# Kernel tuning notes

Hardware: AMD Instinct MI355X
Metric: run time of the kernel (lower is better)

The kernel has to match this reference:

```python
import jax, jax.numpy as jnp
import numpy as np

E = 1024      # embed_size
H = 16        # num_heads
DH = E // H   # head_size = 64
B = 4
T = 2048


def _layernorm(x, g, b, eps=1e-5):
    mu = jnp.mean(x, axis=-1, keepdims=True)
    var = jnp.var(x, axis=-1, keepdims=True)
    return (x - mu) * jax.lax.rsqrt(var + eps) * g + b


def setup_inputs() -> dict:
    key = jax.random.key(0)
    ks = jax.random.split(key, 12)
    s = 0.02
    return {
        "x": jax.random.normal(ks[0], (B, T, E), dtype=jnp.float32),
        "ln1_g": jnp.ones((E,), jnp.float32),
        "ln1_b": jnp.zeros((E,), jnp.float32),
        "Wq": jax.random.normal(ks[1], (H, E, DH), jnp.float32) * s,
        "Wk": jax.random.normal(ks[2], (H, E, DH), jnp.float32) * s,
        "Wv": jax.random.normal(ks[3], (H, E, DH), jnp.float32) * s,
        "Wp": jax.random.normal(ks[4], (E, E), jnp.float32) * s,
        "bp": jnp.zeros((E,), jnp.float32),
        "ln2_g": jnp.ones((E,), jnp.float32),
        "ln2_b": jnp.zeros((E,), jnp.float32),
        "W1": jax.random.normal(ks[5], (E, 4 * E), jnp.float32) * s,
        "b1": jnp.zeros((4 * E,), jnp.float32),
        "W2": jax.random.normal(ks[6], (4 * E, E), jnp.float32) * s,
        "b2": jnp.zeros((E,), jnp.float32),
    }


def reference(x, ln1_g, ln1_b, Wq, Wk, Wv, Wp, bp, ln2_g, ln2_b, W1, b1, W2, b2):
    # --- self-attention branch (pre-LN) ---
    h = _layernorm(x, ln1_g, ln1_b)
    q = jnp.einsum("bte,hed->bhtd", h, Wq)
    k = jnp.einsum("bte,hed->bhtd", h, Wk)
    v = jnp.einsum("bte,hed->bhtd", h, Wv)
    # NOTE: original scales by embed_size**-0.5 (C of the input), not head_size
    scale = jnp.float32(E) ** -0.5
    w = jnp.einsum("bhtd,bhsd->bhts", q, k) * scale  # [B,H,T,T]
    causal = jnp.tril(jnp.ones((T, T), dtype=bool))
    w = jnp.where(causal, w, -jnp.inf)
    w = jax.nn.softmax(w, axis=-1)
    att = jnp.einsum("bhts,bhsd->bhtd", w, v)        # [B,H,T,DH]
    att = jnp.transpose(att, (0, 2, 1, 3)).reshape(B, T, E)  # concat heads
    x = x + att @ Wp + bp
    # --- FFN branch (pre-LN) ---
    h2 = _layernorm(x, ln2_g, ln2_b)
    ff = jax.nn.relu(h2 @ W1 + b1) @ W2 + b2
    return x + ff
```

## Files before the change

### kernel.cpp

```cpp
#include <hip/hip_runtime.h>
#include <stdint.h>

#define DEV __device__ __forceinline__

typedef unsigned short u16;
typedef short s16x8 __attribute__((ext_vector_type(8)));
typedef u16 u16x4 __attribute__((ext_vector_type(4)));
typedef float f32x4 __attribute__((ext_vector_type(4)));

constexpr int Bc = 4, Tc = 2048, Ec = 1024, Hc = 16, DHc = 64, FFc = 4096;

DEV u16 f2bf(float f) {
    union { float f; uint32_t u; } v; v.f = f;
    uint32_t r = v.u + 0x7fffu + ((v.u >> 16) & 1u);
    return (u16)(r >> 16);
}
DEV float bf2f(u16 u) {
    union { uint32_t u; float f; } v; v.u = ((uint32_t)u) << 16;
    return v.f;
}

DEV void gload16(const void* g, void* l) {
    __builtin_amdgcn_global_load_lds((const __attribute__((address_space(1))) void*)g,
                                     (__attribute__((address_space(3))) void*)l, 16, 0, 0);
}

template <typename TIN>
__global__ __launch_bounds__(256) void transpose_conv(const TIN* __restrict__ in,
                                                      u16* __restrict__ out, int R, int C) {
    __shared__ float tile[32][33];
    int bz = blockIdx.z;
    in  += (size_t)bz * R * C;
    out += (size_t)bz * R * C;
    int c0 = blockIdx.x * 32, r0 = blockIdx.y * 32;
    int tx = threadIdx.x, ty = threadIdx.y;
#pragma unroll
    for (int i = 0; i < 4; i++) {
        int r = ty + 8 * i;
        float v;
        if constexpr (sizeof(TIN) == 4) v = ((const float*)in)[(size_t)(r0 + r) * C + c0 + tx];
        else                            v = bf2f(((const u16*)in)[(size_t)(r0 + r) * C + c0 + tx]);
        tile[r][tx] = v;
    }
    __syncthreads();
#pragma unroll
    for (int i = 0; i < 4; i++) {
        int c = ty + 8 * i;
        out[(size_t)(c0 + c) * R + r0 + tx] = f2bf(tile[tx][c]);
    }
}

__global__ __launch_bounds__(256) void ln_kernel(const float* __restrict__ x, const float* __restrict__ g,
                                                 const float* __restrict__ b, u16* __restrict__ out) {
    int row = blockIdx.x;
    const float4* xr = (const float4*)(x + (size_t)row * Ec);
    int t = threadIdx.x;
    float4 v = xr[t];
    float s = v.x + v.y + v.z + v.w;
    float ss = v.x * v.x + v.y * v.y + v.z * v.z + v.w * v.w;
#pragma unroll
    for (int off = 32; off > 0; off >>= 1) { s += __shfl_xor(s, off); ss += __shfl_xor(ss, off); }
    __shared__ float red[8];
    int wid = t >> 6;
    if ((t & 63) == 0) { red[wid] = s; red[4 + wid] = ss; }
    __syncthreads();
    s = red[0] + red[1] + red[2] + red[3];
    ss = red[4] + red[5] + red[6] + red[7];
    float mu = s * (1.f / Ec);
    float rs = rsqrtf(ss * (1.f / Ec) - mu * mu + 1e-5f);
    float4 gv = ((const float4*)g)[t], bv = ((const float4*)b)[t];
    u16x4 o;
    o[0] = f2bf((v.x - mu) * rs * gv.x + bv.x);
    o[1] = f2bf((v.y - mu) * rs * gv.y + bv.y);
    o[2] = f2bf((v.z - mu) * rs * gv.z + bv.z);
    o[3] = f2bf((v.w - mu) * rs * gv.w + bv.w);
    *(u16x4*)(out + (size_t)row * Ec + t * 4) = o;
}

template <int MODE>
__global__ __launch_bounds__(256) void gemm_kernel(const u16* __restrict__ A, const u16* __restrict__ Bt,
                                                   int K, int N,
                                                   u16* __restrict__ o0, u16* __restrict__ o1, u16* __restrict__ o2,
                                                   float* __restrict__ of, const float* __restrict__ bias,
                                                   const float* __restrict__ res) {
    __shared__ u16 As[128 * 32];
    __shared__ u16 Bs[128 * 32];
    int tm = blockIdx.y * 128, tn = blockIdx.x * 128;
    int tid = threadIdx.x;
    int w = tid >> 6, l = tid & 63;
    int wm = w >> 1, wn = w & 1;
    int q16 = l & 15, g = l >> 4;

    f32x4 acc[4][4];
#pragma unroll
    for (int i = 0; i < 4; i++)
#pragma unroll
        for (int j = 0; j < 4; j++) acc[i][j] = {0.f, 0.f, 0.f, 0.f};

    const u16* Aw0 = A + (size_t)(tm + w * 32 + (l >> 2)) * K + (l & 3) * 8;
    const u16* Aw1 = Aw0 + (size_t)16 * K;
    const u16* Bw0 = Bt + (size_t)(tn + w * 32 + (l >> 2)) * K + (l & 3) * 8;
    const u16* Bw1 = Bw0 + (size_t)16 * K;
    u16* Asw = As + (w * 32) * 32;
    u16* Bsw = Bs + (w * 32) * 32;

    for (int k0 = 0; k0 < K; k0 += 32) {
        gload16(Aw0 + k0, Asw);
        gload16(Aw1 + k0, Asw + 16 * 32);
        gload16(Bw0 + k0, Bsw);
        gload16(Bw1 + k0, Bsw + 16 * 32);
        asm volatile("s_waitcnt vmcnt(0)" ::: "memory");
        __syncthreads();
        s16x8 af[4], bf[4];
#pragma unroll
        for (int i = 0; i < 4; i++) {
            af[i] = *(const s16x8*)(As + (wm * 64 + i * 16 + q16) * 32 + g * 8);
            bf[i] = *(const s16x8*)(Bs + (wn * 64 + i * 16 + q16) * 32 + g * 8);
        }
#pragma unroll
        for (int i = 0; i < 4; i++)
#pragma unroll
            for (int j = 0; j < 4; j++)
                acc[i][j] = __builtin_amdgcn_mfma_f32_16x16x32_bf16(af[i], bf[j], acc[i][j], 0, 0, 0);
        __syncthreads();
    }

#pragma unroll
    for (int i = 0; i < 4; i++) {
        int m0 = tm + wm * 64 + i * 16 + g * 4;
#pragma unroll
        for (int j = 0; j < 4; j++) {
            int n = tn + wn * 64 + j * 16 + q16;
            if constexpr (MODE == 0) {
                int tensor = n >> 10, hh = (n >> 6) & 15, d = n & 63;
                if (tensor < 2) {
                    u16* dst = tensor == 0 ? o0 : o1;
#pragma unroll
                    for (int r = 0; r < 4; r++) {
                        int m = m0 + r;
                        int bb = m >> 11, tt = m & 2047;
                        dst[(((size_t)(bb * Hc + hh) * Tc + tt) << 6) + d] = f2bf(acc[i][j][r]);
                    }
                } else {
#pragma unroll
                    for (int r = 0; r < 4; r++) {
                        int m = m0 + r;
                        int bb = m >> 11, tt = m & 2047;
                        o2[((size_t)(bb * Hc + hh) * DHc + d) * Tc + tt] = f2bf(acc[i][j][r]);
                    }
                }
            } else if constexpr (MODE == 1) {
                float bv = bias[n];
#pragma unroll
                for (int r = 0; r < 4; r++) {
                    int m = m0 + r;
                    o0[(size_t)m * N + n] = f2bf(fmaxf(acc[i][j][r] + bv, 0.f));
                }
            } else {
                float bv = bias[n];
#pragma unroll
                for (int r = 0; r < 4; r++) {
                    int m = m0 + r;
                    of[(size_t)m * N + n] = acc[i][j][r] + bv + res[(size_t)m * N + n];
                }
            }
        }
    }
}

__global__ __launch_bounds__(256) void attn_kernel(const u16* __restrict__ q, const u16* __restrict__ k,
                                                   const u16* __restrict__ vt, u16* __restrict__ att) {
    __shared__ u16 Ks[2][64 * 64];
    __shared__ u16 Vs[2][64 * 64];
    __shared__ u16 pt[4][32][72];
    int bh = blockIdx.y;
    int bb = bh >> 4, hh = bh & 15;
    int q0 = (15 - blockIdx.x) * 128;
    int tid = threadIdx.x;
    int w = tid >> 6, l = tid & 63;
    int q16 = l & 15, g = l >> 4;

    const u16* Q  = q  + (size_t)bh * Tc * DHc;
    const u16* Kp = k  + (size_t)bh * Tc * DHc;
    const u16* Vt = vt + (size_t)bh * DHc * Tc;

    int qw = q0 + w * 32;

    s16x8 qf[2][2];
#pragma unroll
    for (int mf = 0; mf < 2; mf++)
#pragma unroll
        for (int c = 0; c < 2; c++)
            qf[mf][c] = *(const s16x8*)(Q + (size_t)(qw + mf * 16 + q16) * DHc + c * 32 + g * 8);

    f32x4 Of[4][2];
#pragma unroll
    for (int i = 0; i < 4; i++)
#pragma unroll
        for (int j = 0; j < 2; j++) Of[i][j] = {0.f, 0.f, 0.f, 0.f};
    float mrun[2] = {-1e30f, -1e30f};
    float lrun[2] = {0.f, 0.f};
    const float scale = 0.03125f;
    int qidx[2] = {qw + q16, qw + 16 + q16};

    int ri = tid >> 3, sl = tid & 7;

    auto stage = [&](int t, int bufi) {
        int s0 = t * 64;
        gload16(Kp + (size_t)(s0 + ri) * DHc + ((sl ^ (ri & 7)) << 3),        &Ks[bufi][w * 512]);
        gload16(Kp + (size_t)(s0 + ri + 32) * DHc + ((sl ^ (ri & 7)) << 3),   &Ks[bufi][2048 + w * 512]);
        gload16(Vt + (size_t)ri * Tc + s0 + ((sl ^ (ri & 7)) << 3),           &Vs[bufi][w * 512]);
        gload16(Vt + (size_t)(ri + 32) * Tc + s0 + ((sl ^ (ri & 7)) << 3),    &Vs[bufi][2048 + w * 512]);
    };

    int nt = q0 / 64 + 2;
    stage(0, 0);
    for (int t = 0; t < nt; ++t) {
        int cur = t & 1;
        if (t + 1 < nt) {
            stage(t + 1, cur ^ 1);
            asm volatile("s_waitcnt vmcnt(4)" ::: "memory");
        } else {
            asm volatile("s_waitcnt vmcnt(0)" ::: "memory");
        }
        __syncthreads();
        int s0 = t * 64;
        if (s0 < qw + 32) {
            const u16* Ksb = &Ks[cur][0];
            const u16* Vsb = &Vs[cur][0];
            s16x8 kf[4][2];
#pragma unroll
            for (int sf = 0; sf < 4; sf++)
#pragma unroll
                for (int c = 0; c < 2; c++)
                    kf[sf][c] = *(const s16x8*)(Ksb + (sf * 16 + q16) * 64 + (((c * 4 + g) ^ (q16 & 7)) << 3));

            f32x4 sacc[4][2];
#pragma unroll
            for (int sf = 0; sf < 4; sf++)
#pragma unroll
                for (int j = 0; j < 2; j++) sacc[sf][j] = {0.f, 0.f, 0.f, 0.f};
#pragma unroll
            for (int sf = 0; sf < 4; sf++)
#pragma unroll
                for (int j = 0; j < 2; j++)
#pragma unroll
                    for (int c = 0; c < 2; c++)
                        sacc[sf][j] = __builtin_amdgcn_mfma_f32_16x16x32_bf16(kf[sf][c], qf[j][c], sacc[sf][j], 0, 0, 0);

#pragma unroll
            for (int qfi = 0; qfi < 2; qfi++) {
                float pv[4][4];
                float tmax = -1e30f;
#pragma unroll
                for (int sf = 0; sf < 4; sf++)
#pragma unroll
                    for (int r = 0; r < 4; r++) {
                        int s = s0 + sf * 16 + g * 4 + r;
                        float val = sacc[sf][qfi][r] * scale;
                        if (s > qidx[qfi]) val = -1e30f;
                        pv[sf][r] = val;
                        tmax = fmaxf(tmax, val);
                    }
                tmax = fmaxf(tmax, __shfl_xor(tmax, 16));
                tmax = fmaxf(tmax, __shfl_xor(tmax, 32));
                float mnew = fmaxf(mrun[qfi], tmax);
                float alpha = __expf(mrun[qfi] - mnew);
                mrun[qfi] = mnew;
                float psum = 0.f;
#pragma unroll
                for (int sf = 0; sf < 4; sf++) {
                    float p0 = __expf(pv[sf][0] - mnew);
                    float p1 = __expf(pv[sf][1] - mnew);
                    float p2 = __expf(pv[sf][2] - mnew);
                    float p3 = __expf(pv[sf][3] - mnew);
                    psum += p0 + p1 + p2 + p3;
                    u16x4 pb;
                    pb[0] = f2bf(p0); pb[1] = f2bf(p1); pb[2] = f2bf(p2); pb[3] = f2bf(p3);
                    *(u16x4*)&pt[w][qfi * 16 + q16][sf * 16 + g * 4] = pb;
                }
                psum += __shfl_xor(psum, 16);
                psum += __shfl_xor(psum, 32);
                lrun[qfi] = lrun[qfi] * alpha + psum;
#pragma unroll
                for (int df = 0; df < 4; df++) {
                    Of[df][qfi][0] *= alpha; Of[df][qfi][1] *= alpha;
                    Of[df][qfi][2] *= alpha; Of[df][qfi][3] *= alpha;
                }
            }

#pragma unroll
            for (int c = 0; c < 2; c++) {
                s16x8 vf[4];
#pragma unroll
                for (int df = 0; df < 4; df++)
                    vf[df] = *(const s16x8*)(Vsb + (df * 16 + q16) * 64 + (((c * 4 + g) ^ (q16 & 7)) << 3));
#pragma unroll
                for (int qfi = 0; qfi < 2; qfi++) {
                    s16x8 pb = *(const s16x8*)&pt[w][qfi * 16 + q16][c * 32 + g * 8];
#pragma unroll
                    for (int df = 0; df < 4; df++)
                        Of[df][qfi] = __builtin_amdgcn_mfma_f32_16x16x32_bf16(vf[df], pb, Of[df][qfi], 0, 0, 0);
                }
            }
        }
        __syncthreads();
    }

#pragma unroll
    for (int qfi = 0; qfi < 2; qfi++) {
        float inv = 1.f / lrun[qfi];
        int tq = qw + qfi * 16 + q16;
#pragma unroll
        for (int df = 0; df < 4; df++) {
            u16x4 o;
            o[0] = f2bf(Of[df][qfi][0] * inv);
            o[1] = f2bf(Of[df][qfi][1] * inv);
            o[2] = f2bf(Of[df][qfi][2] * inv);
            o[3] = f2bf(Of[df][qfi][3] * inv);
            *(u16x4*)(att + ((size_t)(bb * Tc + tq)) * Ec + hh * 64 + df * 16 + g * 4) = o;
        }
    }
}

extern "C" void kernel_launch(void* const* d_in, const int* in_sizes, int n_in,
                              void* d_out, int out_size, void* d_ws, size_t ws_size,
                              hipStream_t stream) {
    (void)in_sizes; (void)n_in; (void)out_size; (void)ws_size;
    const float* x    = (const float*)d_in[0];
    const float* ln1g = (const float*)d_in[1];
    const float* ln1b = (const float*)d_in[2];
    const float* Wq   = (const float*)d_in[3];
    const float* Wk   = (const float*)d_in[4];
    const float* Wv   = (const float*)d_in[5];
    const float* Wp   = (const float*)d_in[6];
    const float* bp   = (const float*)d_in[7];
    const float* ln2g = (const float*)d_in[8];
    const float* ln2b = (const float*)d_in[9];
    const float* W1   = (const float*)d_in[10];
    const float* b1   = (const float*)d_in[11];
    const float* W2   = (const float*)d_in[12];
    const float* b2   = (const float*)d_in[13];
    float* out = (float*)d_out;
    char* ws = (char*)d_ws;

    u16*  wqkvt = (u16*)(ws + 0);
    u16*  wpt   = (u16*)(ws + 6291456);
    u16*  w1t   = (u16*)(ws + 8388608);
    u16*  w2t   = (u16*)(ws + 16777216);
    u16*  h     = (u16*)(ws + 25165824);
    u16*  att   = h;
    u16*  qb    = (u16*)(ws + 41943040);
    u16*  h2    = qb;
    u16*  kb    = (u16*)(ws + 58720256);
    u16*  vtb   = (u16*)(ws + 92274688);
    float* x2   = (float*)(ws + 109051904);
    u16*  ff1   = (u16*)(ws + 142606336);

    dim3 tb(32, 8);
    transpose_conv<float><<<dim3(2, 32, 16), tb, 0, stream>>>(Wq, wqkvt,            1024, 64);
    transpose_conv<float><<<dim3(2, 32, 16), tb, 0, stream>>>(Wk, wqkvt + 1048576,  1024, 64);
    transpose_conv<float><<<dim3(2, 32, 16), tb, 0, stream>>>(Wv, wqkvt + 2097152,  1024, 64);
    transpose_conv<float><<<dim3(32, 32, 1), tb, 0, stream>>>(Wp, wpt, 1024, 1024);
    transpose_conv<float><<<dim3(128, 32, 1), tb, 0, stream>>>(W1, w1t, 1024, 4096);
    transpose_conv<float><<<dim3(32, 128, 1), tb, 0, stream>>>(W2, w2t, 4096, 1024);

    ln_kernel<<<8192, 256, 0, stream>>>(x, ln1g, ln1b, h);

    gemm_kernel<0><<<dim3(24, 64), 256, 0, stream>>>(h, wqkvt, 1024, 3072, qb, kb, vtb, nullptr, nullptr, nullptr);

    attn_kernel<<<dim3(16, 64), 256, 0, stream>>>(qb, kb, vtb, att);

    gemm_kernel<2><<<dim3(8, 64), 256, 0, stream>>>(att, wpt, 1024, 1024, nullptr, nullptr, nullptr, x2, bp, x);

    ln_kernel<<<8192, 256, 0, stream>>>(x2, ln2g, ln2b, h2);

    gemm_kernel<1><<<dim3(32, 64), 256, 0, stream>>>(h2, w1t, 1024, 4096, ff1, nullptr, nullptr, nullptr, b1, nullptr);

    gemm_kernel<2><<<dim3(8, 64), 256, 0, stream>>>(ff1, w2t, 4096, 1024, nullptr, nullptr, nullptr, out, b2, x2);
}
```

Before: 646.5 us.

## Keep attention probabilities in registers, lazy rescale, exp2 softmax, XCD-aware block swizzle

The attention kernel stops writing P through shared memory. It packs probabilities with v_cvt_pk_bf16 and redistributes them via lane shuffles into the MFMA operand layout. It switches to exp2 with a prefolded log2e scale and skips the causal mask on fully visible tiles. Max/rescale updates are lazy and happen only when the new max exceeds the running max by more than 8. It also adds s_setprio around MFMA blocks, launch bounds for 4 waves per SIMD, and XCD-style block swizzling for both the GEMM and attention grids. These aim to cut LDS traffic, exp cost and L2 misses, at the price of extra shuffles and more register pressure.

```diff
diff --git a/kernel.cpp b/kernel.cpp
--- a/kernel.cpp
+++ b/kernel.cpp
@@ -18,6 +18,11 @@
 DEV float bf2f(u16 u) {
     union { uint32_t u; float f; } v; v.u = ((uint32_t)u) << 16;
     return v.f;
+}
+DEV uint32_t cvtpk_bf16(float lo, float hi) {
+    uint32_t r;
+    asm("v_cvt_pk_bf16_f32 %0, %1, %2" : "=v"(r) : "v"(lo), "v"(hi));
+    return r;
 }
 
 DEV void gload16(const void* g, void* l) {
@@ -85,7 +90,10 @@
                                                    const float* __restrict__ res) {
     __shared__ u16 As[128 * 32];
     __shared__ u16 Bs[128 * 32];
-    int tm = blockIdx.y * 128, tn = blockIdx.x * 128;
+    int lin = blockIdx.y * gridDim.x + blockIdx.x;
+    int cpx = (gridDim.x * gridDim.y) >> 3;
+    int swz = (lin & 7) * cpx + (lin >> 3);
+    int tm = (swz / gridDim.x) * 128, tn = (swz % gridDim.x) * 128;
     int tid = threadIdx.x;
     int w = tid >> 6, l = tid & 63;
     int wm = w >> 1, wn = w & 1;
@@ -111,17 +119,17 @@
         gload16(Bw1 + k0, Bsw + 16 * 32);
         asm volatile("s_waitcnt vmcnt(0)" ::: "memory");
         __syncthreads();
-        s16x8 af[4], bf[4];
+        s16x8 af[4], bfr[4];
 #pragma unroll
         for (int i = 0; i < 4; i++) {
-            af[i] = *(const s16x8*)(As + (wm * 64 + i * 16 + q16) * 32 + g * 8);
-            bf[i] = *(const s16x8*)(Bs + (wn * 64 + i * 16 + q16) * 32 + g * 8);
+            af[i]  = *(const s16x8*)(As + (wm * 64 + i * 16 + q16) * 32 + g * 8);
+            bfr[i] = *(const s16x8*)(Bs + (wn * 64 + i * 16 + q16) * 32 + g * 8);
         }
 #pragma unroll
         for (int i = 0; i < 4; i++)
 #pragma unroll
             for (int j = 0; j < 4; j++)
-                acc[i][j] = __builtin_amdgcn_mfma_f32_16x16x32_bf16(af[i], bf[j], acc[i][j], 0, 0, 0);
+                acc[i][j] = __builtin_amdgcn_mfma_f32_16x16x32_bf16(af[i], bfr[j], acc[i][j], 0, 0, 0);
         __syncthreads();
     }
 
@@ -168,17 +176,21 @@
     }
 }
 
-__global__ __launch_bounds__(256) void attn_kernel(const u16* __restrict__ q, const u16* __restrict__ k,
-                                                   const u16* __restrict__ vt, u16* __restrict__ att) {
+__global__ __launch_bounds__(256, 4) void attn_kernel(const u16* __restrict__ q, const u16* __restrict__ k,
+                                                      const u16* __restrict__ vt, u16* __restrict__ att) {
     __shared__ u16 Ks[2][64 * 64];
     __shared__ u16 Vs[2][64 * 64];
-    __shared__ u16 pt[4][32][72];
-    int bh = blockIdx.y;
+    int orig = blockIdx.x;
+    int swz = (orig & 7) * 128 + (orig >> 3);
+    int bh = swz >> 4;
+    int q0 = (15 - (swz & 15)) * 128;
     int bb = bh >> 4, hh = bh & 15;
-    int q0 = (15 - blockIdx.x) * 128;
     int tid = threadIdx.x;
     int w = tid >> 6, l = tid & 63;
     int q16 = l & 15, g = l >> 4;
+    int hig = (g >> 1) & 1;
+    int alane0 = ((g & 1) * 2) * 16 + q16;
+    int alane1 = alane0 + 16;
 
     const u16* Q  = q  + (size_t)bh * Tc * DHc;
     const u16* Kp = k  + (size_t)bh * Tc * DHc;
@@ -200,17 +212,16 @@
         for (int j = 0; j < 2; j++) Of[i][j] = {0.f, 0.f, 0.f, 0.f};
     float mrun[2] = {-1e30f, -1e30f};
     float lrun[2] = {0.f, 0.f};
-    const float scale = 0.03125f;
+    const float scale2 = 0.03125f * 1.44269504f;
     int qidx[2] = {qw + q16, qw + 16 + q16};
 
     int ri = tid >> 3, sl = tid & 7;
-
     auto stage = [&](int t, int bufi) {
         int s0 = t * 64;
-        gload16(Kp + (size_t)(s0 + ri) * DHc + ((sl ^ (ri & 7)) << 3),        &Ks[bufi][w * 512]);
-        gload16(Kp + (size_t)(s0 + ri + 32) * DHc + ((sl ^ (ri & 7)) << 3),   &Ks[bufi][2048 + w * 512]);
-        gload16(Vt + (size_t)ri * Tc + s0 + ((sl ^ (ri & 7)) << 3),           &Vs[bufi][w * 512]);
-        gload16(Vt + (size_t)(ri + 32) * Tc + s0 + ((sl ^ (ri & 7)) << 3),    &Vs[bufi][2048 + w * 512]);
+        gload16(Kp + (size_t)(s0 + ri) * DHc + ((sl ^ (ri & 7)) << 3),      &Ks[bufi][w * 512]);
+        gload16(Kp + (size_t)(s0 + ri + 32) * DHc + ((sl ^ (ri & 7)) << 3), &Ks[bufi][2048 + w * 512]);
+        gload16(Vt + (size_t)ri * Tc + s0 + ((sl ^ (ri & 7)) << 3),         &Vs[bufi][w * 512]);
+        gload16(Vt + (size_t)(ri + 32) * Tc + s0 + ((sl ^ (ri & 7)) << 3),  &Vs[bufi][2048 + w * 512]);
     };
 
     int nt = q0 / 64 + 2;
@@ -240,6 +251,7 @@
             for (int sf = 0; sf < 4; sf++)
 #pragma unroll
                 for (int j = 0; j < 2; j++) sacc[sf][j] = {0.f, 0.f, 0.f, 0.f};
+            __builtin_amdgcn_s_setprio(1);
 #pragma unroll
             for (int sf = 0; sf < 4; sf++)
 #pragma unroll
@@ -247,46 +259,74 @@
 #pragma unroll
                     for (int c = 0; c < 2; c++)
                         sacc[sf][j] = __builtin_amdgcn_mfma_f32_16x16x32_bf16(kf[sf][c], qf[j][c], sacc[sf][j], 0, 0, 0);
-
+            __builtin_amdgcn_s_setprio(0);
+
+            uint32_t paq[2][2][4];
 #pragma unroll
             for (int qfi = 0; qfi < 2; qfi++) {
                 float pv[4][4];
                 float tmax = -1e30f;
-#pragma unroll
-                for (int sf = 0; sf < 4; sf++)
-#pragma unroll
-                    for (int r = 0; r < 4; r++) {
-                        int s = s0 + sf * 16 + g * 4 + r;
-                        float val = sacc[sf][qfi][r] * scale;
-                        if (s > qidx[qfi]) val = -1e30f;
-                        pv[sf][r] = val;
-                        tmax = fmaxf(tmax, val);
-                    }
+                if (s0 + 64 > qw + qfi * 16) {
+#pragma unroll
+                    for (int sf = 0; sf < 4; sf++)
+#pragma unroll
+                        for (int r = 0; r < 4; r++) {
+                            int s = s0 + sf * 16 + g * 4 + r;
+                            float val = sacc[sf][qfi][r] * scale2;
+                            if (s > qidx[qfi]) val = -1e30f;
+                            pv[sf][r] = val;
+                            tmax = fmaxf(tmax, val);
+                        }
+                } else {
+#pragma unroll
+                    for (int sf = 0; sf < 4; sf++)
+#pragma unroll
+                        for (int r = 0; r < 4; r++) {
+                            float val = sacc[sf][qfi][r] * scale2;
+                            pv[sf][r] = val;
+                            tmax = fmaxf(tmax, val);
+                        }
+                }
                 tmax = fmaxf(tmax, __shfl_xor(tmax, 16));
                 tmax = fmaxf(tmax, __shfl_xor(tmax, 32));
-                float mnew = fmaxf(mrun[qfi], tmax);
-                float alpha = __expf(mrun[qfi] - mnew);
-                mrun[qfi] = mnew;
+                if (!__all(tmax <= mrun[qfi] + 8.f)) {
+                    float mnew = fmaxf(mrun[qfi], tmax);
+                    float alpha = exp2f(mrun[qfi] - mnew);
+                    mrun[qfi] = mnew;
+                    lrun[qfi] *= alpha;
+#pragma unroll
+                    for (int df = 0; df < 4; df++) {
+                        Of[df][qfi][0] *= alpha; Of[df][qfi][1] *= alpha;
+                        Of[df][qfi][2] *= alpha; Of[df][qfi][3] *= alpha;
+                    }
+                }
+                float m2 = mrun[qfi];
                 float psum = 0.f;
+                uint32_t Dk[4][2];
 #pragma unroll
                 for (int sf = 0; sf < 4; sf++) {
-                    float p0 = __expf(pv[sf][0] - mnew);
-                    float p1 = __expf(pv[sf][1] - mnew);
-                    float p2 = __expf(pv[sf][2] - mnew);
-                    float p3 = __expf(pv[sf][3] - mnew);
-                    psum += p0 + p1 + p2 + p3;
-                    u16x4 pb;
-                    pb[0] = f2bf(p0); pb[1] = f2bf(p1); pb[2] = f2bf(p2); pb[3] = f2bf(p3);
-                    *(u16x4*)&pt[w][qfi * 16 + q16][sf * 16 + g * 4] = pb;
+                    float p0 = exp2f(pv[sf][0] - m2);
+                    float p1 = exp2f(pv[sf][1] - m2);
+                    float p2 = exp2f(pv[sf][2] - m2);
+                    float p3 = exp2f(pv[sf][3] - m2);
+                    psum += (p0 + p1) + (p2 + p3);
+                    Dk[sf][0] = cvtpk_bf16(p0, p1);
+                    Dk[sf][1] = cvtpk_bf16(p2, p3);
                 }
                 psum += __shfl_xor(psum, 16);
                 psum += __shfl_xor(psum, 32);
-                lrun[qfi] = lrun[qfi] * alpha + psum;
-#pragma unroll
-                for (int df = 0; df < 4; df++) {
-                    Of[df][qfi][0] *= alpha; Of[df][qfi][1] *= alpha;
-                    Of[df][qfi][2] *= alpha; Of[df][qfi][3] *= alpha;
-                }
+                lrun[qfi] += psum;
+#pragma unroll
+                for (int c = 0; c < 2; c++)
+#pragma unroll
+                    for (int kk = 0; kk < 2; kk++) {
+                        int rlo0 = __shfl((int)Dk[c * 2][kk], alane0);
+                        int rhi0 = __shfl((int)Dk[c * 2 + 1][kk], alane0);
+                        paq[qfi][c][kk] = hig ? rhi0 : rlo0;
+                        int rlo1 = __shfl((int)Dk[c * 2][kk], alane1);
+                        int rhi1 = __shfl((int)Dk[c * 2 + 1][kk], alane1);
+                        paq[qfi][c][2 + kk] = hig ? rhi1 : rlo1;
+                    }
             }
 
 #pragma unroll
@@ -295,13 +335,16 @@
 #pragma unroll
                 for (int df = 0; df < 4; df++)
                     vf[df] = *(const s16x8*)(Vsb + (df * 16 + q16) * 64 + (((c * 4 + g) ^ (q16 & 7)) << 3));
+                __builtin_amdgcn_s_setprio(1);
 #pragma unroll
                 for (int qfi = 0; qfi < 2; qfi++) {
-                    s16x8 pb = *(const s16x8*)&pt[w][qfi * 16 + q16][c * 32 + g * 8];
+                    s16x8 pb;
+                    memcpy(&pb, &paq[qfi][c][0], 16);
 #pragma unroll
                     for (int df = 0; df < 4; df++)
                         Of[df][qfi] = __builtin_amdgcn_mfma_f32_16x16x32_bf16(vf[df], pb, Of[df][qfi], 0, 0, 0);
                 }
+                __builtin_amdgcn_s_setprio(0);
             }
         }
         __syncthreads();
@@ -369,7 +412,7 @@
 
     gemm_kernel<0><<<dim3(24, 64), 256, 0, stream>>>(h, wqkvt, 1024, 3072, qb, kb, vtb, nullptr, nullptr, nullptr);
 
-    attn_kernel<<<dim3(16, 64), 256, 0, stream>>>(qb, kb, vtb, att);
+    attn_kernel<<<1024, 256, 0, stream>>>(qb, kb, vtb, att);
 
     gemm_kernel<2><<<dim3(8, 64), 256, 0, stream>>>(att, wpt, 1024, 1024, nullptr, nullptr, nullptr, x2, bp, x);
 
```

Result: slower. 660.6 us (+2.2%).
